# Performance work log

Hardware: AMD Instinct MI355X
Metric: run time of the kernel (lower is better)

The kernel has to match this reference:

```python
import jax, jax.numpy as jnp
import numpy as np

DEPTH = 4
HEADS = 8
DIM = 512
DH = DIM // HEADS          # 64
M_FEAT = 256               # FAVOR+ random features
FF = 4 * DIM               # 2048
EPS_K = 1e-4               # FAVOR+ stabilizer
LN_EPS = 1e-5


def _gorf(rng, m, d):
    # gaussian orthogonal random features (lucidrains default, scaling=0)
    blocks = []
    for _ in range(m // d):
        g = rng.normal(size=(d, d))
        q, _ = np.linalg.qr(g)
        blocks.append(q.T)
    Q = np.concatenate(blocks, axis=0)[:m]
    mult = np.linalg.norm(rng.normal(size=(m, d)), axis=1)
    return (mult[:, None] * Q).astype(np.float32)


def setup_inputs() -> dict:
    rng = np.random.default_rng(0)
    B, T, L = 2, 8, 512
    s = 0.02
    x = rng.normal(size=(B, T, L, DIM)).astype(np.float32)
    proj = np.stack([_gorf(rng, M_FEAT, DH) for _ in range(DEPTH)])  # [depth, m, dh]
    def w(*shape):
        return (rng.normal(size=shape) * s).astype(np.float32)
    inp = {
        "x": jnp.asarray(x),
        "proj": jnp.asarray(proj),
        "ln1_g": jnp.ones((DEPTH, DIM), jnp.float32),
        "ln1_b": jnp.zeros((DEPTH, DIM), jnp.float32),
        "Wqkv": jnp.asarray(w(DEPTH, DIM, 3 * DIM)),
        "bqkv": jnp.zeros((DEPTH, 3 * DIM), jnp.float32),
        "Wo": jnp.asarray(w(DEPTH, DIM, DIM)),
        "bo": jnp.zeros((DEPTH, DIM), jnp.float32),
        "ln2_g": jnp.ones((DEPTH, DIM), jnp.float32),
        "ln2_b": jnp.zeros((DEPTH, DIM), jnp.float32),
        "Wff1": jnp.asarray(w(DEPTH, DIM, FF)),
        "bff1": jnp.zeros((DEPTH, FF), jnp.float32),
        "Wff2": jnp.asarray(w(DEPTH, FF, DIM)),
        "bff2": jnp.zeros((DEPTH, DIM), jnp.float32),
    }
    return inp


def _layer_norm(x, g, b):
    mu = jnp.mean(x, -1, keepdims=True)
    var = jnp.mean(jnp.square(x - mu), -1, keepdims=True)
    return (x - mu) * jax.lax.rsqrt(var + LN_EPS) * g + b


def _softmax_kernel(data, proj, is_query):
    # FAVOR+ positive softmax-kernel features (Performer)
    dh = data.shape[-1]
    dn = dh ** -0.25                       # data normalizer
    ratio = proj.shape[0] ** -0.5
    dd = jnp.einsum("bhnd,md->bhnm", data, proj) * dn
    diag = jnp.sum(jnp.square(data), -1, keepdims=True) * (0.5 * dn * dn)
    if is_query:
        mx = jnp.max(dd, axis=-1, keepdims=True)
    else:
        mx = jnp.max(dd, axis=(-1, -2), keepdims=True)
    return ratio * (jnp.exp(dd - diag - mx) + EPS_K)


def _attention(x, Wqkv, bqkv, Wo, bo, proj):
    B, N, D = x.shape
    qkv = x @ Wqkv + bqkv                                   # [B,N,3D]
    q, k, v = jnp.split(qkv, 3, axis=-1)
    def heads(t):
        return t.reshape(B, N, HEADS, DH).transpose(0, 2, 1, 3)  # [B,H,N,dh]
    q, k, v = heads(q), heads(k), heads(v)
    qp = _softmax_kernel(q, proj, True)                     # [B,H,N,m]
    kp = _softmax_kernel(k, proj, False)
    k_sum = jnp.sum(kp, axis=-2)                            # [B,H,m]
    d_inv = 1.0 / jnp.einsum("bhnm,bhm->bhn", qp, k_sum)
    ctx = jnp.einsum("bhnm,bhnd->bhmd", kp, v)              # [B,H,m,dh]
    out = jnp.einsum("bhmd,bhnm,bhn->bhnd", ctx, qp, d_inv)
    out = out.transpose(0, 2, 1, 3).reshape(B, N, D)
    return out @ Wo + bo


def reference(x, proj, ln1_g, ln1_b, Wqkv, bqkv, Wo, bo, ln2_g, ln2_b, Wff1, bff1, Wff2, bff2):
    B, T, L, D = x.shape
    h = x.reshape(B, T * L, D)
    for i in range(DEPTH):
        a = _attention(_layer_norm(h, ln1_g[i], ln1_b[i]), Wqkv[i], bqkv[i], Wo[i], bo[i], proj[i])
        h = h + a
        f = _layer_norm(h, ln2_g[i], ln2_b[i])
        f = jax.nn.gelu(f @ Wff1[i] + bff1[i], approximate=False) @ Wff2[i] + bff2[i]
        h = h + f
    return h.reshape(B, T, L, D)
```

## Files before the change

### kernel.cpp

```cpp
#include <hip/hip_runtime.h>
#include <math.h>

#define DEPTH 4
#define DMODEL 512
#define DH 64
#define MF 256
#define FFD 2048
#define SEQN 4096
#define NROWS 8192

typedef __bf16 bf16_t;
typedef bf16_t bf16x8 __attribute__((ext_vector_type(8)));
typedef bf16_t bf16x4 __attribute__((ext_vector_type(4)));
typedef bf16_t bf16x2 __attribute__((ext_vector_type(2)));
typedef float f32x4v __attribute__((ext_vector_type(4)));

static constexpr float DN = 0.35355339059327373f;
static constexpr float RATIO = 0.0625f;
static constexpr float EPSK = 1e-4f;

__device__ __forceinline__ float gelu_fast(float x) {
    float z2 = x * (1.5957691216f + 0.0713548162f * x * x);
    return x / (1.0f + __expf(-z2));
}

#define AS1(p) ((const __attribute__((address_space(1))) void*)(p))
#define AS3(p) ((__attribute__((address_space(3))) void*)(p))

template <int N> __device__ __forceinline__ void wait_vmcnt() {
    if constexpr (N == 0) asm volatile("s_waitcnt vmcnt(0)" ::: "memory");
    else if constexpr (N == 1) asm volatile("s_waitcnt vmcnt(1)" ::: "memory");
    else if constexpr (N == 2) asm volatile("s_waitcnt vmcnt(2)" ::: "memory");
    else if constexpr (N == 3) asm volatile("s_waitcnt vmcnt(3)" ::: "memory");
    else if constexpr (N == 4) asm volatile("s_waitcnt vmcnt(4)" ::: "memory");
    else if constexpr (N == 5) asm volatile("s_waitcnt vmcnt(5)" ::: "memory");
    else if constexpr (N == 6) asm volatile("s_waitcnt vmcnt(6)" ::: "memory");
    else if constexpr (N == 8) asm volatile("s_waitcnt vmcnt(8)" ::: "memory");
    else asm volatile("s_waitcnt vmcnt(12)" ::: "memory");
}

__global__ __launch_bounds__(256) void ln_kernel(const float* __restrict__ h,
                                                 const float* __restrict__ g,
                                                 const float* __restrict__ b,
                                                 bf16_t* __restrict__ y) {
    int row = blockIdx.x, tid = threadIdx.x;
    const float* hr = h + (size_t)row * DMODEL;
    float v0 = hr[tid], v1 = hr[tid + 256];
    __shared__ float s_sum[256], s_sq[256];
    s_sum[tid] = v0 + v1;
    s_sq[tid] = v0 * v0 + v1 * v1;
    __syncthreads();
    for (int off = 128; off > 0; off >>= 1) {
        if (tid < off) { s_sum[tid] += s_sum[tid + off]; s_sq[tid] += s_sq[tid + off]; }
        __syncthreads();
    }
    float mu = s_sum[0] * (1.0f / DMODEL);
    float var = s_sq[0] * (1.0f / DMODEL) - mu * mu;
    float rstd = rsqrtf(var + 1e-5f);
    bf16_t* yr = y + (size_t)row * DMODEL;
    yr[tid]       = (bf16_t)((v0 - mu) * rstd * g[tid] + b[tid]);
    yr[tid + 256] = (bf16_t)((v1 - mu) * rstd * g[tid + 256] + b[tid + 256]);
}

__global__ __launch_bounds__(256) void ln_add_kernel(float* __restrict__ h,
                                                     const bf16_t* __restrict__ p,
                                                     const float* __restrict__ g,
                                                     const float* __restrict__ b,
                                                     bf16_t* __restrict__ y) {
    int row = blockIdx.x, tid = threadIdx.x;
    float* hr = h + (size_t)row * DMODEL;
    const bf16_t* pr = p + (size_t)row * DMODEL;
    float2 hv = *(const float2*)(hr + 2 * tid);
    bf16x2 pv = *(const bf16x2*)(pr + 2 * tid);
    float v0 = hv.x + (float)pv[0];
    float v1 = hv.y + (float)pv[1];
    float2 outv; outv.x = v0; outv.y = v1;
    *(float2*)(hr + 2 * tid) = outv;
    __shared__ float s_sum[256], s_sq[256];
    s_sum[tid] = v0 + v1;
    s_sq[tid] = v0 * v0 + v1 * v1;
    __syncthreads();
    for (int off = 128; off > 0; off >>= 1) {
        if (tid < off) { s_sum[tid] += s_sum[tid + off]; s_sq[tid] += s_sq[tid + off]; }
        __syncthreads();
    }
    float mu = s_sum[0] * (1.0f / DMODEL);
    float var = s_sq[0] * (1.0f / DMODEL) - mu * mu;
    float rstd = rsqrtf(var + 1e-5f);
    bf16x2 ov;
    ov[0] = (bf16_t)((v0 - mu) * rstd * g[2 * tid] + b[2 * tid]);
    ov[1] = (bf16_t)((v1 - mu) * rstd * g[2 * tid + 1] + b[2 * tid + 1]);
    *(bf16x2*)(y + (size_t)row * DMODEL + 2 * tid) = ov;
}

__global__ __launch_bounds__(256) void add_kernel(float* __restrict__ h,
                                                  const bf16_t* __restrict__ p) {
    size_t i = ((size_t)blockIdx.x * 256 + threadIdx.x) * 4;
    float4 hv = *(const float4*)(h + i);
    bf16x4 pv = *(const bf16x4*)(p + i);
    hv.x += (float)pv[0]; hv.y += (float)pv[1];
    hv.z += (float)pv[2]; hv.w += (float)pv[3];
    *(float4*)(h + i) = hv;
}

__global__ __launch_bounds__(256) void wconv_all(const float* __restrict__ Wqkv,
                                                 const float* __restrict__ Wo,
                                                 const float* __restrict__ Wff1,
                                                 const float* __restrict__ Wff2,
                                                 bf16_t* __restrict__ wslot) {
    __shared__ float t[32][33];
    int layer = blockIdx.y;
    int bid = blockIdx.x;
    const float* W; bf16_t* Wt; int K, N, nx, lb;
    bf16_t* slot = wslot + (size_t)layer * 3407872;
    if (bid < 768)       { W = Wqkv + (size_t)layer * 786432;  Wt = slot;           K = 512;  N = 1536; nx = 48; lb = bid; }
    else if (bid < 1024) { W = Wo   + (size_t)layer * 262144;  Wt = slot + 786432;  K = 512;  N = 512;  nx = 16; lb = bid - 768; }
    else if (bid < 2048) { W = Wff1 + (size_t)layer * 1048576; Wt = slot + 1048576; K = 512;  N = 2048; nx = 64; lb = bid - 1024; }
    else                 { W = Wff2 + (size_t)layer * 1048576; Wt = slot + 2097152; K = 2048; N = 512;  nx = 16; lb = bid - 2048; }
    int n0 = (lb % nx) * 32, k0 = (lb / nx) * 32;
    int tx = threadIdx.x & 31, ty = threadIdx.x >> 5;
#pragma unroll
    for (int i = 0; i < 32; i += 8)
        t[ty + i][tx] = W[(size_t)(k0 + ty + i) * N + n0 + tx];
    __syncthreads();
#pragma unroll
    for (int i = 0; i < 32; i += 8)
        Wt[(size_t)(n0 + ty + i) * K + k0 + tx] = (bf16_t)t[tx][ty + i];
}

__global__ __launch_bounds__(256) void pconv_kernel(const float* __restrict__ proj,
                                                    bf16_t* __restrict__ projb) {
    int i = (blockIdx.x * 256 + threadIdx.x) * 4;
    float4 v = *(const float4*)(proj + i);
    bf16x4 o;
    o[0] = (bf16_t)v.x; o[1] = (bf16_t)v.y; o[2] = (bf16_t)v.z; o[3] = (bf16_t)v.w;
    *(bf16x4*)(projb + i) = o;
}

template <int BM, int BN, int BK, int P, int ACT, int RES, int WF, int WB, int QKVE>
__global__ __launch_bounds__(256) void gemm_pipe(const bf16_t* __restrict__ A,
                                                 const bf16_t* __restrict__ Bt,
                                                 const float* __restrict__ bias,
                                                 float* __restrict__ Cf,
                                                 bf16_t* __restrict__ Cb,
                                                 bf16_t* __restrict__ Vt,
                                                 int N, int K) {
    static_assert(BK == 32, "BK fixed at 32 (KS==1)");
    constexpr int MR = BM / 2 / 16;
    constexpr int NR = BN / 2 / 16;
    constexpr int CH = BK / 8;
    constexpr int SWZ = CH - 1;
    constexpr int TILE = (BM + BN) * BK;
    constexpr int L = TILE / 8 / 256;
    __shared__ __attribute__((aligned(16))) bf16_t smem[P * TILE];
    int tid = threadIdx.x;
    int wv = tid >> 6, ln = tid & 63;
    int gx = gridDim.x;
    int lin = blockIdx.y * gx + blockIdx.x;
    int per = (gx * gridDim.y) >> 3;
    int orig = (lin & 7) * per + (lin >> 3);
    int m0 = (orig / gx) * BM, n0 = (orig % gx) * BN;
    int wr = (wv >> 1) * (MR * 16), wc = (wv & 1) * (NR * 16);
    int lr = ln & 15, kq8 = ln >> 4;
    int nsteps = K / BK;

    const bf16_t* gsrc[L];
    int ldst[L];
#pragma unroll
    for (int i = 0; i < L; i++) {
        int c = i * 256 + tid;
        int cb = i * 256 + (tid & ~63);
        bool inA = (c < BM * CH);
        int cc = inA ? c : c - BM * CH;
        int row = cc / CH, ch = cc % CH;
        const bf16_t* mat = inA ? A : Bt;
        int r0 = inA ? m0 : n0;
        int chs = ch ^ ((row ^ (row >> 2)) & SWZ);
        gsrc[i] = mat + (size_t)(r0 + row) * K + chs * 8;
        ldst[i] = cb * 8;
    }
    auto stage = [&](int tile, int sb) {
        int k0 = tile * BK;
        bf16_t* dst = smem + sb * TILE;
#pragma unroll
        for (int i = 0; i < L; i++)
            __builtin_amdgcn_global_load_lds(AS1(gsrc[i] + k0), AS3(dst + ldst[i]), 16, 0, 0);
    };

    int aoff[MR], boff[NR];
#pragma unroll
    for (int m = 0; m < MR; m++) {
        int row = wr + m * 16 + lr;
        aoff[m] = (row * CH + (kq8 ^ ((row ^ (row >> 2)) & SWZ))) * 8;
    }
#pragma unroll
    for (int n = 0; n < NR; n++) {
        int row = wc + n * 16 + lr;
        boff[n] = BM * BK + (row * CH + (kq8 ^ ((row ^ (row >> 2)) & SWZ))) * 8;
    }

    f32x4v acc[MR][NR] = {};
#pragma unroll
    for (int p = 0; p < P - 1; ++p) stage(p, p);

    int cur = 0;
    for (int t = 0; t < nsteps; ++t) {
        int rem = nsteps - 1 - t;
        if (rem >= P - 2) wait_vmcnt<(P - 2) * L>();
        else if constexpr (P >= 4) {
            if (rem == 1) wait_vmcnt<L>(); else wait_vmcnt<0>();
        } else wait_vmcnt<0>();
        __builtin_amdgcn_s_barrier();
        asm volatile("" ::: "memory");
        if (t + P - 1 < nsteps) {
            int sb = cur - 1; if (sb < 0) sb = P - 1;
            stage(t + P - 1, sb);
        }
        const bf16_t* base = smem + cur * TILE;
        bf16x8 af[MR], bfr[NR];
#pragma unroll
        for (int m = 0; m < MR; m++) af[m] = *(const bf16x8*)&base[aoff[m]];
#pragma unroll
        for (int n = 0; n < NR; n++) bfr[n] = *(const bf16x8*)&base[boff[n]];
        __builtin_amdgcn_s_setprio(1);
#pragma unroll
        for (int m = 0; m < MR; m++)
#pragma unroll
            for (int n = 0; n < NR; n++)
                acc[m][n] = __builtin_amdgcn_mfma_f32_16x16x32_bf16(af[m], bfr[n], acc[m][n], 0, 0, 0);
        __builtin_amdgcn_s_setprio(0);
        cur = (cur + 1 == P) ? 0 : cur + 1;
    }
    int rq = (ln >> 4) * 4;
    if (WB || QKVE) {
        __syncthreads();
        bf16_t* T = smem;
        constexpr int S = BN + 8;
#pragma unroll
        for (int n = 0; n < NR; n++) {
            int col = wc + n * 16 + lr;
            float bcol = bias[n0 + col];
#pragma unroll
            for (int m = 0; m < MR; m++) {
#pragma unroll
                for (int r = 0; r < 4; r++) {
                    int row = wr + m * 16 + rq + r;
                    float v = acc[m][n][r] + bcol;
                    if (ACT == 1) v = gelu_fast(v);
                    int cs = (col & 7) | ((((col >> 3) ^ (row >> 3)) & (BN / 8 - 1)) << 3);
                    T[row * S + cs] = (bf16_t)v;
                }
            }
        }
        __syncthreads();
        if (!QKVE || n0 < 1024) {
            int ldc = QKVE ? 1024 : N;
#pragma unroll
            for (int i = 0; i < BM * BN / 8 / 256; i++) {
                int e = i * 2048 + tid * 8;
                int row = e / BN, c0 = e % BN;
                int ch = ((c0 >> 3) ^ (row >> 3)) & (BN / 8 - 1);
                bf16x8 v = *(const bf16x8*)&T[row * S + ch * 8];
                *(bf16x8*)&Cb[(size_t)(m0 + row) * ldc + n0 + c0] = v;
            }
        } else {
#pragma unroll
            for (int i = 0; i < BM * BN / 8 / 256; i++) {
                int u = i * 256 + tid;
                int d = u & (BN - 1), nb8 = (u / BN) * 8;
                bf16x8 v;
#pragma unroll
                for (int j = 0; j < 8; j++) {
                    int row = nb8 + j;
                    int cs = (d & 7) | ((((d >> 3) ^ (row >> 3)) & (BN / 8 - 1)) << 3);
                    v[j] = T[row * S + cs];
                }
                int gcol = n0 + d;
                int hh2 = (gcol >> 6) & 7, dd2 = gcol & 63;
                int grow = m0 + nb8;
                int bb = grow >> 12, nn = grow & 4095;
                *(bf16x8*)&Vt[(((size_t)bb * 8 + hh2) * 64 + dd2) * 4096 + nn] = v;
            }
        }
    } else {
#pragma unroll
        for (int n = 0; n < NR; n++) {
            int col = n0 + wc + n * 16 + lr;
            float bcol = bias[col];
#pragma unroll
            for (int m = 0; m < MR; m++) {
#pragma unroll
                for (int r = 0; r < 4; r++) {
                    int row = m0 + wr + m * 16 + rq + r;
                    float v = acc[m][n][r] + bcol;
                    if (ACT == 1) v = gelu_fast(v);
                    size_t idx = (size_t)row * N + col;
                    if (RES) Cf[idx] += v;
                    else Cf[idx] = v;
                }
            }
        }
    }
}

__global__ __launch_bounds__(256) void feat_kernel(const bf16_t* __restrict__ qkvb,
                                                   const bf16_t* __restrict__ projb,
                                                   bf16_t* __restrict__ outp,
                                                   float* __restrict__ ksum_part) {
    int bid = blockIdx.x;
    int bh = bid >> 5, tile = bid & 31;
    int b = bh >> 3, hh = bh & 7;
    int tid = threadIdx.x, wv = tid >> 6, ln = tid & 63;
    __shared__ __attribute__((aligned(16))) bf16_t As[128 * 64];
    __shared__ __attribute__((aligned(16))) bf16_t Bs[256 * 64];
    __shared__ float diag_s[128];
    __shared__ float ksp_s[256];
    int n0 = tile * 128;
    int qoff = 512 + hh * 64;
    int lrow8 = ln >> 3;
    int lchunk = ((ln & 7) ^ (lrow8 & 7)) * 8;
#pragma unroll
    for (int i = 0; i < 4; i++) {
        int e = wv * 4 + i;
        size_t src = (size_t)(b * SEQN + n0 + e * 8 + lrow8) * 1024 + qoff + lchunk;
        __builtin_amdgcn_global_load_lds(AS1(qkvb + src), AS3(&As[e * 512]), 16, 0, 0);
    }
#pragma unroll
    for (int i = 0; i < 8; i++) {
        int e = wv * 8 + i;
        size_t src = (size_t)(e * 8 + lrow8) * 64 + lchunk;
        __builtin_amdgcn_global_load_lds(AS1(projb + src), AS3(&Bs[e * 512]), 16, 0, 0);
    }
    __syncthreads();
    if (tid < 128) {
        float s = 0.f;
#pragma unroll
        for (int c = 0; c < 8; c++) {
            bf16x8 v = *(const bf16x8*)&As[tid * 64 + ((c ^ (tid & 7)) * 8)];
#pragma unroll
            for (int j = 0; j < 8; j++) { float f = (float)v[j]; s += f * f; }
        }
        diag_s[tid] = s * (0.5f * DN * DN);
    }
    int wr = (wv >> 1) * 64, wc = (wv & 1) * 128;
    int lr = ln & 15, kg = ln >> 4, rq = kg * 4;
    f32x4v acc[4][8] = {};
#pragma unroll
    for (int ks = 0; ks < 2; ks++) {
        int g = ks * 4 + kg;
        bf16x8 af[4], bfv[8];
#pragma unroll
        for (int m = 0; m < 4; m++) {
            int row = wr + m * 16 + lr;
            af[m] = *(const bf16x8*)&As[row * 64 + ((g ^ (row & 7)) * 8)];
        }
#pragma unroll
        for (int n = 0; n < 8; n++) {
            int row = wc + n * 16 + lr;
            bfv[n] = *(const bf16x8*)&Bs[row * 64 + ((g ^ (row & 7)) * 8)];
        }
#pragma unroll
        for (int m = 0; m < 4; m++)
#pragma unroll
            for (int n = 0; n < 8; n++)
                acc[m][n] = __builtin_amdgcn_mfma_f32_16x16x32_bf16(af[m], bfv[n], acc[m][n], 0, 0, 0);
    }
    __syncthreads();
    float sj[8] = {};
#pragma unroll
    for (int m = 0; m < 4; m++) {
#pragma unroll
        for (int n = 0; n < 8; n++) {
            int col = wc + n * 16 + lr;
            bf16x4 pk;
#pragma unroll
            for (int r = 0; r < 4; r++) {
                int row = wr + m * 16 + rq + r;
                float val = RATIO * (__expf(acc[m][n][r] * DN - diag_s[row]) + EPSK);
                pk[r] = (bf16_t)val;
                sj[n] += val;
            }
            *(bf16x4*)&outp[((size_t)bh * MF + col) * 4096 + n0 + wr + m * 16 + rq] = pk;
        }
    }
#pragma unroll
    for (int n = 0; n < 8; n++) {
        sj[n] += __shfl_xor(sj[n], 16);
        sj[n] += __shfl_xor(sj[n], 32);
    }
    if (wv < 2 && ln < 16) {
#pragma unroll
        for (int n = 0; n < 8; n++) ksp_s[wc + n * 16 + ln] = sj[n];
    }
    __syncthreads();
    if (wv >= 2 && ln < 16) {
#pragma unroll
        for (int n = 0; n < 8; n++) ksp_s[wc + n * 16 + ln] += sj[n];
    }
    __syncthreads();
    ksum_part[(size_t)bid * 256 + tid] = ksp_s[tid];
}

__global__ __launch_bounds__(256) void ctx_gemm(const bf16_t* __restrict__ KPt,
                                                const bf16_t* __restrict__ Vt,
                                                float* __restrict__ part) {
    int bh = blockIdx.y;
    int mtile = blockIdx.x & 1, kc = blockIdx.x >> 1;
    int m0 = mtile * 128, nb = kc * 512;
    int tid = threadIdx.x, wv = tid >> 6, ln = tid & 63;
    __shared__ __attribute__((aligned(16))) bf16_t As[128 * 64];
    __shared__ __attribute__((aligned(16))) bf16_t Bs[64 * 64];
    int lrow8 = ln >> 3;
    int lchunk = ((ln & 7) ^ (lrow8 & 7)) * 8;
    int lr = ln & 15, kg = ln >> 4, rq = kg * 4;
    int wr = wv * 32;
    f32x4v acc[2][4] = {};
    for (int kt = 0; kt < 8; kt++) {
        int noff = nb + kt * 64;
        __syncthreads();
#pragma unroll
        for (int i = 0; i < 4; i++) {
            int e = wv * 4 + i;
            __builtin_amdgcn_global_load_lds(
                AS1(KPt + ((size_t)bh * MF + m0 + e * 8 + lrow8) * 4096 + noff + lchunk),
                AS3(&As[e * 512]), 16, 0, 0);
        }
#pragma unroll
        for (int i = 0; i < 2; i++) {
            int e = wv * 2 + i;
            __builtin_amdgcn_global_load_lds(
                AS1(Vt + ((size_t)bh * 64 + e * 8 + lrow8) * 4096 + noff + lchunk),
                AS3(&Bs[e * 512]), 16, 0, 0);
        }
        __syncthreads();
#pragma unroll
        for (int ks = 0; ks < 2; ks++) {
            int g = ks * 4 + kg;
            bf16x8 af[2], bfv[4];
#pragma unroll
            for (int m = 0; m < 2; m++) {
                int row = wr + m * 16 + lr;
                af[m] = *(const bf16x8*)&As[row * 64 + ((g ^ (row & 7)) * 8)];
            }
#pragma unroll
            for (int n = 0; n < 4; n++) {
                int row = n * 16 + lr;
                bfv[n] = *(const bf16x8*)&Bs[row * 64 + ((g ^ (row & 7)) * 8)];
            }
#pragma unroll
            for (int m = 0; m < 2; m++)
#pragma unroll
                for (int n = 0; n < 4; n++)
                    acc[m][n] = __builtin_amdgcn_mfma_f32_16x16x32_bf16(af[m], bfv[n], acc[m][n], 0, 0, 0);
        }
    }
#pragma unroll
    for (int m = 0; m < 2; m++)
#pragma unroll
        for (int n = 0; n < 4; n++)
#pragma unroll
            for (int r = 0; r < 4; r++)
                part[((size_t)(kc * 16 + bh) * MF + m0 + wr + m * 16 + rq + r) * 64 + n * 16 + lr] =
                    acc[m][n][r];
}

__global__ __launch_bounds__(256) void ctx_reduce_kernel(const float* __restrict__ part,
                                                         const float* __restrict__ ksum_part,
                                                         bf16_t* __restrict__ ctx_t,
                                                         float* __restrict__ ksum) {
    int bh = blockIdx.x;
    for (int it = 0; it < 64; it++) {
        int idx = it * 256 + threadIdx.x;
        int m = idx >> 6, d = idx & 63;
        float s = 0.f;
#pragma unroll
        for (int kc = 0; kc < 8; kc++)
            s += part[(size_t)(kc * 16 + bh) * 16384 + idx];
        ctx_t[((size_t)bh * 64 + d) * MF + m] = (bf16_t)s;
    }
    {
        float s = 0.f;
#pragma unroll
        for (int t = 0; t < 32; t++)
            s += ksum_part[((size_t)bh * 32 + t) * 256 + threadIdx.x];
        ksum[bh * MF + threadIdx.x] = s;
    }
}

__global__ __launch_bounds__(256) void qfused_kernel(const bf16_t* __restrict__ qkvb,
                                                     const bf16_t* __restrict__ projb,
                                                     const bf16_t* __restrict__ ctx_t,
                                                     const float* __restrict__ ksumb,
                                                     bf16_t* __restrict__ abuf) {
    int bid = blockIdx.x;
    int bh = bid >> 5, tile = bid & 31;
    int b = bh >> 3, hh = bh & 7;
    int tid = threadIdx.x, wv = tid >> 6, ln = tid & 63;
    __shared__ __attribute__((aligned(16))) bf16_t Qs[128 * 64];
    __shared__ __attribute__((aligned(16))) bf16_t Ps[256 * 64];
    __shared__ __attribute__((aligned(16))) bf16_t Cs[64 * 256];
    __shared__ float diag_s[128];
    __shared__ float dsum_s[128];
    int n0 = tile * 128;
    int lrow8 = ln >> 3;
    int lchunk = ((ln & 7) ^ (lrow8 & 7)) * 8;
#pragma unroll
    for (int i = 0; i < 4; i++) {
        int e = wv * 4 + i;
        size_t src = (size_t)(b * SEQN + n0 + e * 8 + lrow8) * 1024 + hh * 64 + lchunk;
        __builtin_amdgcn_global_load_lds(AS1(qkvb + src), AS3(&Qs[e * 512]), 16, 0, 0);
    }
#pragma unroll
    for (int i = 0; i < 8; i++) {
        int e = wv * 8 + i;
        size_t src = (size_t)(e * 8 + lrow8) * 64 + lchunk;
        __builtin_amdgcn_global_load_lds(AS1(projb + src), AS3(&Ps[e * 512]), 16, 0, 0);
    }
#pragma unroll
    for (int i = 0; i < 8; i++) {
        int c = i * 256 + tid;
        int cb = i * 256 + (tid & ~63);
        int crow = c >> 5, cch = c & 31;
        size_t src = ((size_t)bh * 64 + crow) * 256 + (size_t)(cch ^ (crow & 7)) * 8;
        __builtin_amdgcn_global_load_lds(AS1(ctx_t + src), AS3(Cs + (size_t)cb * 8), 16, 0, 0);
    }
    int wr = (wv >> 1) * 64, wc = (wv & 1) * 128;
    int lr = ln & 15, kg = ln >> 4, rq = kg * 4;
    float ksum_r[8];
#pragma unroll
    for (int n = 0; n < 8; n++) ksum_r[n] = ksumb[bh * MF + wc + n * 16 + lr];
    __syncthreads();
    if (tid < 128) {
        float s = 0.f;
#pragma unroll
        for (int c = 0; c < 8; c++) {
            bf16x8 v = *(const bf16x8*)&Qs[tid * 64 + ((c ^ (tid & 7)) * 8)];
#pragma unroll
            for (int j = 0; j < 8; j++) { float f = (float)v[j]; s += f * f; }
        }
        diag_s[tid] = s * (0.5f * DN * DN);
    }
    f32x4v acc[4][8] = {};
#pragma unroll
    for (int ks = 0; ks < 2; ks++) {
        int g = ks * 4 + kg;
        bf16x8 af[4], bfv[8];
#pragma unroll
        for (int m = 0; m < 4; m++) {
            int row = wr + m * 16 + lr;
            af[m] = *(const bf16x8*)&Qs[row * 64 + ((g ^ (row & 7)) * 8)];
        }
#pragma unroll
        for (int n = 0; n < 8; n++) {
            int row = wc + n * 16 + lr;
            bfv[n] = *(const bf16x8*)&Ps[row * 64 + ((g ^ (row & 7)) * 8)];
        }
#pragma unroll
        for (int m = 0; m < 4; m++)
#pragma unroll
            for (int n = 0; n < 8; n++)
                acc[m][n] = __builtin_amdgcn_mfma_f32_16x16x32_bf16(af[m], bfv[n], acc[m][n], 0, 0, 0);
    }
    __syncthreads();
    float dsum_p[4][4];
#pragma unroll
    for (int m = 0; m < 4; m++) {
#pragma unroll
        for (int r = 0; r < 4; r++) {
            int row = wr + m * 16 + rq + r;
            float dg = diag_s[row];
            float ds = 0.f;
#pragma unroll
            for (int n = 0; n < 8; n++) {
                float val = RATIO * (__expf(acc[m][n][r] * DN - dg) + EPSK);
                acc[m][n][r] = val;
                ds += val * ksum_r[n];
            }
            dsum_p[m][r] = ds;
        }
    }
#pragma unroll
    for (int m = 0; m < 4; m++)
#pragma unroll
        for (int r = 0; r < 4; r++) {
#pragma unroll
            for (int mask = 1; mask < 16; mask <<= 1)
                dsum_p[m][r] += __shfl_xor(dsum_p[m][r], mask);
        }
    if ((wv & 1) == 0 && lr == 0) {
#pragma unroll
        for (int m = 0; m < 4; m++)
#pragma unroll
            for (int r = 0; r < 4; r++)
                dsum_s[wr + m * 16 + rq + r] = dsum_p[m][r];
    }
    __syncthreads();
    if ((wv & 1) == 1 && lr == 0) {
#pragma unroll
        for (int m = 0; m < 4; m++)
#pragma unroll
            for (int r = 0; r < 4; r++) {
                int row = wr + m * 16 + rq + r;
                dsum_s[row] = 1.0f / (dsum_s[row] + dsum_p[m][r]);
            }
    }
    __syncthreads();
    f32x4v acc_o[4][2] = {};
#pragma unroll
    for (int h = 0; h < 2; h++) {
        if ((wv & 1) == h) {
#pragma unroll
            for (int m = 0; m < 4; m++)
#pragma unroll
                for (int n = 0; n < 8; n++)
#pragma unroll
                    for (int r = 0; r < 4; r++) {
                        int row = wr + m * 16 + rq + r;
                        int ml = n * 16 + lr;
                        Ps[row * 128 + (((ml >> 3) ^ (row & 7)) * 8) + (ml & 7)] =
                            (bf16_t)acc[m][n][r];
                    }
        }
        __syncthreads();
#pragma unroll
        for (int ku = 0; ku < 4; ku++) {
            int g = ku * 4 + kg;
            bf16x8 af[4], bfv[2];
#pragma unroll
            for (int m = 0; m < 4; m++) {
                int row = wr + m * 16 + lr;
                af[m] = *(const bf16x8*)&Ps[row * 128 + ((g ^ (row & 7)) * 8)];
            }
#pragma unroll
            for (int n = 0; n < 2; n++) {
                int rowd = (wv & 1) * 32 + n * 16 + lr;
                int ch = (h * 16 + g) ^ (rowd & 7);
                bfv[n] = *(const bf16x8*)&Cs[(rowd * 32 + ch) * 8];
            }
#pragma unroll
            for (int m = 0; m < 4; m++)
#pragma unroll
                for (int n = 0; n < 2; n++)
                    acc_o[m][n] = __builtin_amdgcn_mfma_f32_16x16x32_bf16(af[m], bfv[n], acc_o[m][n], 0, 0, 0);
        }
        __syncthreads();
    }
#pragma unroll
    for (int m = 0; m < 4; m++) {
#pragma unroll
        for (int r = 0; r < 4; r++) {
            int rowl = wr + m * 16 + rq + r;
            float di = dsum_s[rowl];
            size_t obase = ((size_t)(b * SEQN + n0 + rowl)) * DMODEL + hh * 64;
#pragma unroll
            for (int n = 0; n < 2; n++) {
                int d = (wv & 1) * 32 + n * 16 + lr;
                abuf[obase + d] = (bf16_t)(acc_o[m][n][r] * di);
            }
        }
    }
}

extern "C" void kernel_launch(void* const* d_in, const int* in_sizes, int n_in,
                              void* d_out, int out_size, void* d_ws, size_t ws_size,
                              hipStream_t stream) {
    const float* x     = (const float*)d_in[0];
    const float* proj  = (const float*)d_in[1];
    const float* ln1_g = (const float*)d_in[2];
    const float* ln1_b = (const float*)d_in[3];
    const float* Wqkv  = (const float*)d_in[4];
    const float* bqkv  = (const float*)d_in[5];
    const float* Wo    = (const float*)d_in[6];
    const float* bo    = (const float*)d_in[7];
    const float* ln2_g = (const float*)d_in[8];
    const float* ln2_b = (const float*)d_in[9];
    const float* Wff1  = (const float*)d_in[10];
    const float* bff1  = (const float*)d_in[11];
    const float* Wff2  = (const float*)d_in[12];
    const float* bff2  = (const float*)d_in[13];

    float* h = (float*)d_out;
    char* ws = (char*)d_ws;
    bf16_t* KPt   = (bf16_t*)(ws);
    bf16_t* ybf   = (bf16_t*)(ws);
    bf16_t* pWo   = (bf16_t*)(ws + 8388608);
    bf16_t* pFF2  = (bf16_t*)(ws + 16777216);
    bf16_t* qkvb  = (bf16_t*)(ws + 33554432);
    bf16_t* abufb = (bf16_t*)(ws + 50331648);
    float*  ctx_part  = (float*)(ws + 58720256);
    float*  ksum_part = (float*)(ws + 67108864);
    bf16_t* ffmidb    = (bf16_t*)(ws + 50331648);
    bf16_t* Vt    = (bf16_t*)(ws + 83886080);
    bf16_t* projb = (bf16_t*)(ws + 92274688);
    bf16_t* ctx_t = (bf16_t*)(ws + 92405760);
    float*  ksumb = (float*)(ws + 92930048);
    bf16_t* wbase = (bf16_t*)(ws + 93061120);
    const size_t WSLOT = 3407872;
    bool hoist = ws_size >= (size_t)93061120 + 4 * 6815744;

    hipMemcpyAsync(h, x, (size_t)NROWS * DMODEL * sizeof(float),
                   hipMemcpyDeviceToDevice, stream);
    pconv_kernel<<<64, 256, 0, stream>>>(proj, projb);
    if (hoist)
        wconv_all<<<dim3(3072, 4), 256, 0, stream>>>(Wqkv, Wo, Wff1, Wff2, wbase);

    for (int i = 0; i < DEPTH; i++) {
        const bf16_t* pj = projb + (size_t)i * MF * DH;
        if (!hoist)
            wconv_all<<<dim3(3072, 1), 256, 0, stream>>>(
                Wqkv + (size_t)i * 786432, Wo + (size_t)i * 262144,
                Wff1 + (size_t)i * 1048576, Wff2 + (size_t)i * 1048576, wbase);
        bf16_t* wl = wbase + (hoist ? (size_t)i * WSLOT : 0);
        bf16_t* wq_t = wl;
        bf16_t* wo_t = wl + 786432;
        bf16_t* w1_t = wl + 1048576;
        bf16_t* w2_t = wl + 2097152;

        if (i == 0)
            ln_kernel<<<NROWS, 256, 0, stream>>>(h, ln1_g, ln1_b, ybf);
        else
            ln_add_kernel<<<NROWS, 256, 0, stream>>>(h, pFF2, ln1_g + i * DMODEL,
                                                     ln1_b + i * DMODEL, ybf);
        gemm_pipe<128, 64, 32, 3, 0, 0, 0, 0, 1>
            <<<dim3(1536 / 64, NROWS / 128), 256, 0, stream>>>(
            ybf, wq_t, bqkv + i * 1536, nullptr, qkvb, Vt, 1536, 512);
        feat_kernel<<<512, 256, 0, stream>>>(qkvb, pj, KPt, ksum_part);
        ctx_gemm<<<dim3(16, 16), 256, 0, stream>>>(KPt, Vt, ctx_part);
        ctx_reduce_kernel<<<16, 256, 0, stream>>>(ctx_part, ksum_part, ctx_t, ksumb);
        qfused_kernel<<<512, 256, 0, stream>>>(qkvb, pj, ctx_t, ksumb, abufb);
        gemm_pipe<128, 64, 32, 3, 0, 0, 0, 1, 0>
            <<<dim3(512 / 64, NROWS / 128), 256, 0, stream>>>(
            abufb, wo_t, bo + i * DMODEL, nullptr, pWo, nullptr, 512, 512);

        ln_add_kernel<<<NROWS, 256, 0, stream>>>(h, pWo, ln2_g + i * DMODEL,
                                                 ln2_b + i * DMODEL, ybf);
        gemm_pipe<128, 64, 32, 3, 1, 0, 0, 1, 0>
            <<<dim3(2048 / 64, NROWS / 128), 256, 0, stream>>>(
            ybf, w1_t, bff1 + i * FFD, nullptr, ffmidb, nullptr, 2048, 512);
        gemm_pipe<128, 64, 32, 3, 0, 0, 0, 1, 0>
            <<<dim3(512 / 64, NROWS / 128), 256, 0, stream>>>(
            ffmidb, w2_t, bff2 + i * DMODEL, nullptr, pFF2, nullptr, 512, 2048);
    }
    add_kernel<<<4096, 256, 0, stream>>>(h, pFF2);
}
```

Baseline: 789.6 us.

## Stage feature-map output through LDS for coalesced stores; drop initial residual copy

The feature kernel no longer writes transposed bf16x4 fragments straight to global memory. It converts the exponentiated accumulators in registers, transposes them through the reused A/B shared buffer in two halves, and writes full 16-byte contiguous rows to global memory. Separately, the initial device-to-device copy of x into the residual buffer is removed: layer 0 reads x directly, and ln_add_kernel takes separate input and output residual pointers. The changes target uncoalesced scattered stores and an extra 16 MB copy, at the cost of extra LDS traffic and two more barriers per feature block.

```diff
diff --git a/kernel.cpp b/kernel.cpp
--- a/kernel.cpp
+++ b/kernel.cpp
@@ -62,20 +62,21 @@
     yr[tid + 256] = (bf16_t)((v1 - mu) * rstd * g[tid + 256] + b[tid + 256]);
 }
 
-__global__ __launch_bounds__(256) void ln_add_kernel(float* __restrict__ h,
+__global__ __launch_bounds__(256) void ln_add_kernel(const float* __restrict__ hin,
+                                                     float* __restrict__ hout,
                                                      const bf16_t* __restrict__ p,
                                                      const float* __restrict__ g,
                                                      const float* __restrict__ b,
                                                      bf16_t* __restrict__ y) {
     int row = blockIdx.x, tid = threadIdx.x;
-    float* hr = h + (size_t)row * DMODEL;
+    const float* hr = hin + (size_t)row * DMODEL;
     const bf16_t* pr = p + (size_t)row * DMODEL;
     float2 hv = *(const float2*)(hr + 2 * tid);
     bf16x2 pv = *(const bf16x2*)(pr + 2 * tid);
     float v0 = hv.x + (float)pv[0];
     float v1 = hv.y + (float)pv[1];
     float2 outv; outv.x = v0; outv.y = v1;
-    *(float2*)(hr + 2 * tid) = outv;
+    *(float2*)(hout + (size_t)row * DMODEL + 2 * tid) = outv;
     __shared__ float s_sum[256], s_sq[256];
     s_sum[tid] = v0 + v1;
     s_sq[tid] = v0 * v0 + v1 * v1;
@@ -311,8 +312,9 @@
     int bh = bid >> 5, tile = bid & 31;
     int b = bh >> 3, hh = bh & 7;
     int tid = threadIdx.x, wv = tid >> 6, ln = tid & 63;
-    __shared__ __attribute__((aligned(16))) bf16_t As[128 * 64];
-    __shared__ __attribute__((aligned(16))) bf16_t Bs[256 * 64];
+    __shared__ __attribute__((aligned(16))) bf16_t AsBs[128 * 64 + 256 * 64];
+    bf16_t* As = AsBs;
+    bf16_t* Bs = AsBs + 128 * 64;
     __shared__ float diag_s[128];
     __shared__ float ksp_s[256];
     int n0 = tile * 128;
@@ -371,16 +373,13 @@
     for (int m = 0; m < 4; m++) {
 #pragma unroll
         for (int n = 0; n < 8; n++) {
-            int col = wc + n * 16 + lr;
-            bf16x4 pk;
 #pragma unroll
             for (int r = 0; r < 4; r++) {
                 int row = wr + m * 16 + rq + r;
                 float val = RATIO * (__expf(acc[m][n][r] * DN - diag_s[row]) + EPSK);
-                pk[r] = (bf16_t)val;
+                acc[m][n][r] = val;
                 sj[n] += val;
             }
-            *(bf16x4*)&outp[((size_t)bh * MF + col) * 4096 + n0 + wr + m * 16 + rq] = pk;
         }
     }
 #pragma unroll
@@ -399,6 +398,33 @@
     }
     __syncthreads();
     ksum_part[(size_t)bid * 256 + tid] = ksp_s[tid];
+    bf16_t* T = AsBs;
+#pragma unroll
+    for (int hf = 0; hf < 2; hf++) {
+        if ((wv & 1) == hf) {
+#pragma unroll
+            for (int n = 0; n < 8; n++) {
+                int mm = n * 16 + lr;
+#pragma unroll
+                for (int m = 0; m < 4; m++) {
+                    int nnb = wr + m * 16 + rq;
+                    bf16x4 v;
+#pragma unroll
+                    for (int r = 0; r < 4; r++) v[r] = (bf16_t)acc[m][n][r];
+                    *(bf16x4*)&T[mm * 136 + nnb] = v;
+                }
+            }
+        }
+        __syncthreads();
+#pragma unroll
+        for (int i = 0; i < 8; i++) {
+            int u = i * 256 + tid;
+            int mm = u >> 4, nc = u & 15;
+            bf16x8 v = *(const bf16x8*)&T[mm * 136 + nc * 8];
+            *(bf16x8*)&outp[((size_t)bh * MF + hf * 128 + mm) * 4096 + n0 + nc * 8] = v;
+        }
+        __syncthreads();
+    }
 }
 
 __global__ __launch_bounds__(256) void ctx_gemm(const bf16_t* __restrict__ KPt,
@@ -698,8 +724,6 @@
     const size_t WSLOT = 3407872;
     bool hoist = ws_size >= (size_t)93061120 + 4 * 6815744;
 
-    hipMemcpyAsync(h, x, (size_t)NROWS * DMODEL * sizeof(float),
-                   hipMemcpyDeviceToDevice, stream);
     pconv_kernel<<<64, 256, 0, stream>>>(proj, projb);
     if (hoist)
         wconv_all<<<dim3(3072, 4), 256, 0, stream>>>(Wqkv, Wo, Wff1, Wff2, wbase);
@@ -717,9 +741,9 @@
         bf16_t* w2_t = wl + 2097152;
 
         if (i == 0)
-            ln_kernel<<<NROWS, 256, 0, stream>>>(h, ln1_g, ln1_b, ybf);
+            ln_kernel<<<NROWS, 256, 0, stream>>>(x, ln1_g, ln1_b, ybf);
         else
-            ln_add_kernel<<<NROWS, 256, 0, stream>>>(h, pFF2, ln1_g + i * DMODEL,
+            ln_add_kernel<<<NROWS, 256, 0, stream>>>(h, h, pFF2, ln1_g + i * DMODEL,
                                                      ln1_b + i * DMODEL, ybf);
         gemm_pipe<128, 64, 32, 3, 0, 0, 0, 0, 1>
             <<<dim3(1536 / 64, NROWS / 128), 256, 0, stream>>>(
@@ -732,7 +756,8 @@
             <<<dim3(512 / 64, NROWS / 128), 256, 0, stream>>>(
             abufb, wo_t, bo + i * DMODEL, nullptr, pWo, nullptr, 512, 512);
 
-        ln_add_kernel<<<NROWS, 256, 0, stream>>>(h, pWo, ln2_g + i * DMODEL,
+        ln_add_kernel<<<NROWS, 256, 0, stream>>>(i == 0 ? x : h, h, pWo,
+                                                 ln2_g + i * DMODEL,
                                                  ln2_b + i * DMODEL, ybf);
         gemm_pipe<128, 64, 32, 3, 1, 0, 0, 1, 0>
             <<<dim3(2048 / 64, NROWS / 128), 256, 0, stream>>>(
```

New measurement: 786.1 us. No clear change (-0.4%).
